# Optimization experiments

Measured on AMD Instinct MI355X. Metric: run time of the kernel, lower is better.

The kernel has to match this reference:

```python
import jax, jax.numpy as jnp
import numpy as np

EPS = 1e-7
K_IN, K_HID, K_OUT = 1.0, 1.1, 1.2
N_NODES, N_EDGES, IN_DIM, HID = 50000, 400000, 1024, 1024


def _expmap0(u, k):
    # u: tangent at origin with time component 0; u[:, 1:] are spatial coords
    sqrtK = jnp.sqrt(k)
    us = u[:, 1:]
    un = jnp.maximum(jnp.linalg.norm(us, axis=1, keepdims=True), EPS)
    t = un / sqrtK
    return jnp.concatenate([sqrtK * jnp.cosh(t), sqrtK * jnp.sinh(t) * us / un], axis=1)


def _logmap0(x, k):
    sqrtK = jnp.sqrt(k)
    x0, xs = x[:, 0:1], x[:, 1:]
    xn = jnp.maximum(jnp.linalg.norm(xs, axis=1, keepdims=True), EPS)
    theta = jnp.maximum(x0 / sqrtK, 1.0 + EPS)
    d = sqrtK * jnp.arccosh(theta)
    return jnp.concatenate([jnp.zeros_like(x0), d * xs / xn], axis=1)


def _proj(x, k):
    # re-fix the time component so <x,x>_L = -k
    xs = x[:, 1:]
    x0 = jnp.sqrt(k + jnp.sum(xs * xs, axis=1, keepdims=True))
    return jnp.concatenate([x0, xs], axis=1)


def _centroid(m, k):
    # Lorentzian centroid normalization: sqrt(k) * m / sqrt(|<m,m>_L|)
    l_inner = jnp.sum(m[:, 1:] ** 2, axis=1, keepdims=True) - m[:, 0:1] ** 2
    denom = jnp.sqrt(jnp.maximum(jnp.abs(l_inner), EPS))
    return jnp.sqrt(k) * m / denom


def _lgcn_conv(x, W, b, edge_src, edge_dst, edge_w, k_in, k_out):
    n = x.shape[0]
    # Lorentzian linear: logmap0 -> spatial matmul + bias -> expmap0
    u = _logmap0(x, k_in)[:, 1:]                      # [N, in_f]
    mx = u @ W.T + b                                  # [N, out_f-1]
    h = _expmap0(jnp.concatenate([jnp.zeros_like(mx[:, :1]), mx], axis=1), k_in)
    # sparse neighborhood aggregation + Lorentzian centroid
    msgs = edge_w[:, None] * h[edge_src]              # [E, out_f]
    m = jax.ops.segment_sum(msgs, edge_dst, num_segments=n)
    h = _centroid(m, k_in)
    # Lorentzian activation: relu in tangent space, re-exp on output manifold
    t = jax.nn.relu(_logmap0(h, k_in))                # time comp stays 0
    return _proj(_expmap0(t, k_out), k_out)


def setup_inputs() -> dict:
    key = jax.random.key(0)
    ks = jax.random.split(key, 8)
    x = jax.random.normal(ks[0], (N_NODES, IN_DIM), jnp.float32) * 0.01
    edge_src = jax.random.randint(ks[1], (N_EDGES,), 0, N_NODES, jnp.int32)
    edge_dst = jax.random.randint(ks[2], (N_EDGES,), 0, N_NODES, jnp.int32)
    edge_w = jax.random.uniform(ks[3], (N_EDGES,), jnp.float32)
    W1 = jax.random.normal(ks[4], (HID - 1, IN_DIM), jnp.float32) * 0.02
    b1 = jax.random.normal(ks[5], (HID - 1,), jnp.float32) * 0.01
    W2 = jax.random.normal(ks[6], (HID - 1, HID - 1), jnp.float32) * 0.02
    b2 = jax.random.normal(ks[7], (HID - 1,), jnp.float32) * 0.01
    return {"x": x, "edge_src": edge_src, "edge_dst": edge_dst, "edge_w": edge_w,
            "W1": W1, "b1": b1, "W2": W2, "b2": b2}


def reference(x, edge_src, edge_dst, edge_w, W1, b1, W2, b2):
    # encode(): prepend zero time coord, proj_tan0 (already 0), expmap0, proj
    x = jnp.concatenate([jnp.zeros_like(x[:, :1]), x], axis=1)  # [N, IN_DIM+1]
    xh = _proj(_expmap0(x, K_IN), K_IN)
    x1 = _lgcn_conv(xh, W1, b1, edge_src, edge_dst, edge_w, K_IN, K_HID)
    y = _lgcn_conv(x1, W2, b2, edge_src, edge_dst, edge_w, K_HID, K_OUT)
    return y
```

## Files before the change

### kernel.cpp

```cpp
#include <hip/hip_runtime.h>
#include <math.h>

#define EPSF 1e-7f
#define KPAD 1024
#define M_PAD 50176
#define NWG2 784

typedef __attribute__((ext_vector_type(8))) short bf16x8;
typedef __attribute__((ext_vector_type(4))) float f32x4;
typedef __attribute__((ext_vector_type(4))) unsigned short us4;
typedef __attribute__((ext_vector_type(8))) unsigned short us8;

__device__ inline unsigned short f2bf(float f) {
  unsigned u = __float_as_uint(f);
  return (unsigned short)((u + 0x7FFFu + ((u >> 16) & 1u)) >> 16);
}
__device__ inline float bf2f(unsigned short s) {
  return __uint_as_float(((unsigned)s) << 16);
}

__device__ inline float block_sum256(float v, float* s4) {
#pragma unroll
  for (int o = 32; o > 0; o >>= 1) v += __shfl_down(v, o);
  int lane = threadIdx.x & 63, w = threadIdx.x >> 6;
  __syncthreads();
  if (lane == 0) s4[w] = v;
  __syncthreads();
  return s4[0] + s4[1] + s4[2] + s4[3];
}

__device__ inline void gload_lds16(const void* g, void* l) {
  __builtin_amdgcn_global_load_lds((const __attribute__((address_space(1))) void*)g,
                                   (__attribute__((address_space(3))) void*)l, 16, 0, 0);
}

__global__ __launch_bounds__(256) void cvt_rows_bf16(const float* __restrict__ x,
                                                     unsigned short* __restrict__ o) {
  int i = blockIdx.x, t = threadIdx.x;
  float4 v = *(const float4*)(x + (size_t)i * 1024 + 4 * t);
  us4 u = {f2bf(v.x), f2bf(v.y), f2bf(v.z), f2bf(v.w)};
  *(us4*)(o + (size_t)i * 1024 + 4 * t) = u;
}

__global__ __launch_bounds__(256) void cvt_w_bf16(const float* __restrict__ W,
                                                  unsigned short* __restrict__ o,
                                                  int rows, int cols) {
  int r = blockIdx.x, t = threadIdx.x;
  int c0 = 4 * t;
  us4 u;
#pragma unroll
  for (int j = 0; j < 4; ++j) {
    int c = c0 + j;
    float v = (r < rows && c < cols) ? W[(size_t)r * cols + c] : 0.0f;
    u[j] = f2bf(v);
  }
  *(us4*)(o + (size_t)r * 1024 + c0) = u;
}

__global__ __launch_bounds__(512, 2) void gemm_bt256(const unsigned short* __restrict__ A,
                                                     const unsigned short* __restrict__ B,
                                                     const float* __restrict__ bias,
                                                     unsigned short* __restrict__ C) {
  __shared__ unsigned short lA[2 * 2 * 8192];
  __shared__ unsigned short lB[2 * 2 * 8192];
  const int wg = blockIdx.x;
  const int swz = (wg & 7) * 98 + (wg >> 3);
  const int bm = swz >> 2, bn = swz & 3;
  const int tid = threadIdx.x;
  const int wave = tid >> 6, lane = tid & 63;
  const int wr = wave >> 2, wc = wave & 3;
  const int fr = lane & 15, fg = lane >> 4;

  const unsigned short* Abase = A + (size_t)bm * 256 * KPAD;
  const unsigned short* Bbase = B + (size_t)bn * 256 * KPAD;

  const int aHalf = wr * 8192;
  const int bHalf = (wc >> 1) * 8192;
  const int lrB0 = (wc & 1) * 64;
  int ps[2];
#pragma unroll
  for (int s = 0; s < 2; ++s) ps[s] = (((s << 2) + fg) ^ (fr & 7)) << 3;

  const int sRow8 = lane >> 3;
  const int sDst = wave * 512 + lane * 8;
  const int sGran = ((lane & 7) ^ sRow8) << 3;

  f32x4 acc[8][4];
#pragma unroll
  for (int m = 0; m < 8; ++m)
#pragma unroll
    for (int n2 = 0; n2 < 4; ++n2) acc[m][n2] = (f32x4)0.0f;

  bf16x8 af[4][2], bf[4][2];

  auto STAGE_A = [&](int t, int h) {
    const int p = t & 1;
#pragma unroll
    for (int q = 0; q < 2; ++q) {
      int row = h * 128 + q * 64 + wave * 8 + sRow8;
      gload_lds16(Abase + (size_t)row * KPAD + t * 64 + sGran,
                  &lA[p * 16384 + h * 8192 + q * 4096 + sDst]);
    }
  };
  auto STAGE_B = [&](int t, int h) {
    const int p = t & 1;
#pragma unroll
    for (int q = 0; q < 2; ++q) {
      int row = h * 128 + q * 64 + wave * 8 + sRow8;
      gload_lds16(Bbase + (size_t)row * KPAD + t * 64 + sGran,
                  &lB[p * 16384 + h * 8192 + q * 4096 + sDst]);
    }
  };
  auto LDA4 = [&](int p, int mg) {
#pragma unroll
    for (int mi = 0; mi < 4; ++mi) {
      int ro = p * 16384 + aHalf + ((mg * 4 + mi) * 16 + fr) * 64;
#pragma unroll
      for (int s = 0; s < 2; ++s) af[mi][s] = *(const bf16x8*)&lA[ro + ps[s]];
    }
  };
  auto LDB2 = [&](int p, int ng) {
#pragma unroll
    for (int ni = 0; ni < 2; ++ni) {
      int ro = p * 16384 + bHalf + (lrB0 + (ng * 2 + ni) * 16 + fr) * 64;
#pragma unroll
      for (int s = 0; s < 2; ++s) bf[ng * 2 + ni][s] = *(const bf16x8*)&lB[ro + ps[s]];
    }
  };
  auto MM = [&](int mq, int nq) {
    __builtin_amdgcn_s_setprio(1);
#pragma unroll
    for (int mi = 0; mi < 4; ++mi)
#pragma unroll
      for (int ni = 0; ni < 2; ++ni)
#pragma unroll
        for (int s = 0; s < 2; ++s)
          acc[mq * 4 + mi][nq * 2 + ni] = __builtin_amdgcn_mfma_f32_16x16x32_bf16(
              af[mi][s], bf[nq * 2 + ni][s], acc[mq * 4 + mi][nq * 2 + ni], 0, 0, 0);
    __builtin_amdgcn_s_setprio(0);
  };
#define BAR() __builtin_amdgcn_s_barrier()

  STAGE_B(0, 0); STAGE_B(0, 1); STAGE_A(0, 0); STAGE_A(0, 1);
  STAGE_B(1, 0); STAGE_B(1, 1); STAGE_A(1, 0);
  asm volatile("s_waitcnt vmcnt(6)" ::: "memory");
  BAR();

#pragma unroll 1
  for (int it = 0; it < 7; ++it) {
    const int t0 = 2 * it, t1 = t0 + 1;
    LDA4(0, 0); LDB2(0, 0);
    STAGE_A(t1, 1);
    BAR(); MM(0, 0); BAR();
    LDB2(0, 1);
    BAR(); MM(0, 1); BAR();
    LDA4(0, 1);
    STAGE_B(t0 + 2, 0);
    BAR(); MM(1, 0); BAR();
    STAGE_B(t0 + 2, 1); STAGE_A(t0 + 2, 0);
    asm volatile("s_waitcnt vmcnt(6)" ::: "memory");
    BAR(); MM(1, 1); BAR();
    LDA4(1, 0); LDB2(1, 0);
    STAGE_A(t0 + 2, 1);
    BAR(); MM(0, 0); BAR();
    LDB2(1, 1);
    BAR(); MM(0, 1); BAR();
    LDA4(1, 1);
    STAGE_B(t1 + 2, 0);
    BAR(); MM(1, 0); BAR();
    STAGE_B(t1 + 2, 1); STAGE_A(t1 + 2, 0);
    asm volatile("s_waitcnt vmcnt(6)" ::: "memory");
    BAR(); MM(1, 1); BAR();
  }

  asm volatile("s_waitcnt vmcnt(0)" ::: "memory");
  BAR();
#pragma unroll
  for (int p = 0; p < 2; ++p) {
    LDA4(p, 0); LDB2(p, 0); MM(0, 0);
    LDB2(p, 1); MM(0, 1);
    LDA4(p, 1); MM(1, 0); MM(1, 1);
  }
#undef BAR

  const int crow0 = bm * 256 + wr * 128;
  const int ccol0 = bn * 256 + wc * 64;
#pragma unroll
  for (int m = 0; m < 8; ++m) {
#pragma unroll
    for (int n2 = 0; n2 < 4; ++n2) {
      int col = ccol0 + n2 * 16 + fr;
      float bv = (col < 1023) ? bias[col] : 0.0f;
      int row0 = crow0 + m * 16 + fg * 4;
      unsigned short* cp = C + (size_t)row0 * 1024 + col;
#pragma unroll
      for (int j = 0; j < 4; ++j) cp[(size_t)j * 1024] = f2bf(acc[m][n2][j] + bv);
    }
  }
}

__global__ __launch_bounds__(256) void row_scale(unsigned short* __restrict__ raw,
                                                 float* __restrict__ sc_tab, float sqrtK) {
  __shared__ float s4[4];
  int i = blockIdx.x, t = threadIdx.x;
  const us4 v = *(const us4*)(raw + (size_t)i * 1024 + 4 * t);
  float f0 = bf2f(v[0]), f1 = bf2f(v[1]), f2 = bf2f(v[2]), f3 = bf2f(v[3]);
  if (t == 255) f3 = 0.0f;
  float ss = block_sum256(f0 * f0 + f1 * f1 + f2 * f2 + f3 * f3, s4);
  float un = fmaxf(sqrtf(ss), EPSF);
  float tt = un / sqrtK;
  float e = expf(tt);
  float ch = 0.5f * (e + 1.0f / e), sh = 0.5f * (e - 1.0f / e);
  float h0 = sqrtK * ch, sc = sqrtK * sh / un;
  if (t == 0) sc_tab[i] = sc;
  if (t == 255) raw[(size_t)i * 1024 + 1023] = f2bf(h0 / sc);
}

__global__ __launch_bounds__(256) void deg_count(const int* __restrict__ ed, int* __restrict__ cnt,
                                                 int nE) {
  int i = blockIdx.x * 256 + threadIdx.x;
  if (i < nE) atomicAdd(&cnt[ed[i]], 1);
}

__global__ __launch_bounds__(256) void scan1(const int* __restrict__ cnt, int* __restrict__ excl,
                                             int* __restrict__ bsum, int n) {
  __shared__ int s[256];
  int t = threadIdx.x;
  int i = blockIdx.x * 256 + t;
  int v = (i < n) ? cnt[i] : 0;
  s[t] = v;
  __syncthreads();
#pragma unroll
  for (int o = 1; o < 256; o <<= 1) {
    int add = (t >= o) ? s[t - o] : 0;
    __syncthreads();
    s[t] += add;
    __syncthreads();
  }
  if (i < n) excl[i] = s[t] - v;
  if (t == 255) bsum[blockIdx.x] = s[t];
}

__global__ __launch_bounds__(256) void scan2(int* __restrict__ bsum, int* __restrict__ boff,
                                             int nb) {
  __shared__ int s[256];
  int t = threadIdx.x;
  int v = (t < nb) ? bsum[t] : 0;
  s[t] = v;
  __syncthreads();
#pragma unroll
  for (int o = 1; o < 256; o <<= 1) {
    int add = (t >= o) ? s[t - o] : 0;
    __syncthreads();
    s[t] += add;
    __syncthreads();
  }
  if (t < nb) boff[t] = s[t] - v;
}

__global__ __launch_bounds__(256) void scan3(int* __restrict__ excl, const int* __restrict__ boff,
                                             int* __restrict__ rowstart, int* __restrict__ fill,
                                             int n, int nE) {
  int i = blockIdx.x * 256 + threadIdx.x;
  if (i < n) {
    int v = excl[i] + boff[blockIdx.x];
    rowstart[i] = v;
    fill[i] = v;
  }
  if (i == 0) rowstart[n] = nE;
}

__global__ __launch_bounds__(256) void bucket_fill(const int* __restrict__ es,
                                                   const int* __restrict__ ed,
                                                   const float* __restrict__ ew,
                                                   int* __restrict__ fill,
                                                   int2* __restrict__ sedge, int nE) {
  int i = blockIdx.x * 256 + threadIdx.x;
  if (i < nE) {
    int d = ed[i];
    int pos = atomicAdd(&fill[d], 1);
    sedge[pos] = make_int2(es[i], __float_as_int(ew[i]));
  }
}

__device__ inline void gather_row(const unsigned short* __restrict__ h,
                                  const float* __restrict__ sc,
                                  const int2* __restrict__ sedge, int j0, int j1, int t,
                                  float* acc) {
  int j = j0;
  for (; j + 4 <= j1; j += 4) {
    int2 e0 = sedge[j], e1 = sedge[j + 1], e2 = sedge[j + 2], e3 = sedge[j + 3];
    float w0 = __int_as_float(e0.y) * sc[e0.x];
    float w1 = __int_as_float(e1.y) * sc[e1.x];
    float w2 = __int_as_float(e2.y) * sc[e2.x];
    float w3 = __int_as_float(e3.y) * sc[e3.x];
    us8 v0 = *(const us8*)(h + (size_t)e0.x * 1024 + 8 * t);
    us8 v1 = *(const us8*)(h + (size_t)e1.x * 1024 + 8 * t);
    us8 v2 = *(const us8*)(h + (size_t)e2.x * 1024 + 8 * t);
    us8 v3 = *(const us8*)(h + (size_t)e3.x * 1024 + 8 * t);
#pragma unroll
    for (int q = 0; q < 8; ++q) {
      acc[q] += w0 * bf2f(v0[q]);
      acc[q] += w1 * bf2f(v1[q]);
      acc[q] += w2 * bf2f(v2[q]);
      acc[q] += w3 * bf2f(v3[q]);
    }
  }
  for (; j < j1; ++j) {
    int2 e = sedge[j];
    float w = __int_as_float(e.y) * sc[e.x];
    us8 v = *(const us8*)(h + (size_t)e.x * 1024 + 8 * t);
#pragma unroll
    for (int q = 0; q < 8; ++q) acc[q] += w * bf2f(v[q]);
  }
}

__global__ __launch_bounds__(256) void gather_centroid_tangent(
    const unsigned short* __restrict__ h, const float* __restrict__ sc,
    const int* __restrict__ rs, const int2* __restrict__ sedge,
    unsigned short* __restrict__ u16, float sqrtK, int n) {
  __shared__ float s4[4];
  __shared__ float sm0[2];
  int g = threadIdx.x >> 7;
  int t = threadIdx.x & 127;
  int i = blockIdx.x * 2 + g;
  bool alive = (i < n);
  int j0 = alive ? rs[i] : 0, j1 = alive ? rs[i + 1] : 0;
  float acc[8] = {0.f, 0.f, 0.f, 0.f, 0.f, 0.f, 0.f, 0.f};
  gather_row(h, sc, sedge, j0, j1, t, acc);
  if (t == 127) sm0[g] = acc[7];
  __syncthreads();
  float m0 = sm0[g];
  if (t == 127) acc[7] = 0.0f;
  float ssl = 0.f;
#pragma unroll
  for (int q = 0; q < 8; ++q) ssl += acc[q] * acc[q];
#pragma unroll
  for (int o = 32; o > 0; o >>= 1) ssl += __shfl_down(ssl, o);
  int lane = threadIdx.x & 63, wv = threadIdx.x >> 6;
  if (lane == 0) s4[wv] = ssl;
  __syncthreads();
  float ss = s4[2 * g] + s4[2 * g + 1];

  float l = ss - m0 * m0;
  float denom = sqrtf(fmaxf(fabsf(l), EPSF));
  float c = sqrtK / denom;
  float xn = fmaxf(c * sqrtf(ss), EPSF);
  float theta = fmaxf(m0 / denom, 1.0f + EPSF);
  float d = sqrtK * acoshf(theta);
  float f = c * (d / xn);
  us8 u;
#pragma unroll
  for (int q = 0; q < 8; ++q) u[q] = f2bf(fmaxf(acc[q], 0.0f) * f);
  if (t == 127) u[7] = 0;
  if (alive) *(us8*)(u16 + (size_t)i * 1024 + 8 * t) = u;
}

__global__ __launch_bounds__(256) void gather_centroid_final(
    const unsigned short* __restrict__ h, const float* __restrict__ sc,
    const int* __restrict__ rs, const int2* __restrict__ sedge, float* __restrict__ y,
    float sqrtKin, float sqrtKout, int n) {
  __shared__ float s4[4];
  __shared__ float s4b[4];
  __shared__ float sm0[2];
  int g = threadIdx.x >> 7;
  int t = threadIdx.x & 127;
  int i = blockIdx.x * 2 + g;
  bool alive = (i < n);
  int j0 = alive ? rs[i] : 0, j1 = alive ? rs[i + 1] : 0;
  float acc[8] = {0.f, 0.f, 0.f, 0.f, 0.f, 0.f, 0.f, 0.f};
  gather_row(h, sc, sedge, j0, j1, t, acc);
  if (t == 127) sm0[g] = acc[7];
  __syncthreads();
  float m0 = sm0[g];
  if (t == 127) acc[7] = 0.0f;
  float ssl = 0.f;
#pragma unroll
  for (int q = 0; q < 8; ++q) ssl += acc[q] * acc[q];
#pragma unroll
  for (int o = 32; o > 0; o >>= 1) ssl += __shfl_down(ssl, o);
  int lane = threadIdx.x & 63, wv = threadIdx.x >> 6;
  if (lane == 0) s4[wv] = ssl;
  __syncthreads();
  float ss = s4[2 * g] + s4[2 * g + 1];

  float l = ss - m0 * m0;
  float denom = sqrtf(fmaxf(fabsf(l), EPSF));
  float c = sqrtKin / denom;
  float xn = fmaxf(c * sqrtf(ss), EPSF);
  float theta = fmaxf(m0 / denom, 1.0f + EPSF);
  float d = sqrtKin * acoshf(theta);
  float f = c * (d / xn);
  float o_[8];
#pragma unroll
  for (int q = 0; q < 8; ++q) o_[q] = fmaxf(acc[q], 0.0f) * f;
  if (t == 127) o_[7] = 0.0f;
  float ss2l = 0.f;
#pragma unroll
  for (int q = 0; q < 8; ++q) ss2l += o_[q] * o_[q];
#pragma unroll
  for (int o = 32; o > 0; o >>= 1) ss2l += __shfl_down(ss2l, o);
  if (lane == 0) s4b[wv] = ss2l;
  __syncthreads();
  float ss2 = s4b[2 * g] + s4b[2 * g + 1];

  float un = fmaxf(sqrtf(ss2), EPSF);
  float tt = un / sqrtKout;
  float e = expf(tt);
  float ch = 0.5f * (e + 1.0f / e), sh = 0.5f * (e - 1.0f / e);
  float y0 = sqrtKout * ch, scale = sqrtKout * sh / un;
  if (alive) {
    float* yr = y + (size_t)i * 1024;
    int c0 = 8 * t;
#pragma unroll
    for (int q = 0; q < 8; ++q) {
      int col = c0 + q;
      if (col < 1023) yr[1 + col] = scale * o_[q];
    }
    if (t == 0) yr[0] = y0;
  }
}

extern "C" void kernel_launch(void* const* d_in, const int* in_sizes, int n_in,
                              void* d_out, int out_size, void* d_ws, size_t ws_size,
                              hipStream_t stream) {
  const float* x = (const float*)d_in[0];
  const int* es = (const int*)d_in[1];
  const int* ed = (const int*)d_in[2];
  const float* ew = (const float*)d_in[3];
  const float* W1 = (const float*)d_in[4];
  const float* b1 = (const float*)d_in[5];
  const float* W2 = (const float*)d_in[6];
  const float* b2 = (const float*)d_in[7];
  float* y = (float*)d_out;

  const int n = in_sizes[0] / 1024;
  const int nE = in_sizes[1];
  const int NB = (n + 255) / 256;
  const int EB = (nE + 255) / 256;

  char* ws = (char*)d_ws;
  size_t off = 0;
  auto alloc = [&](size_t bytes) {
    void* p = ws + off;
    off += (bytes + 255) & ~(size_t)255;
    return p;
  };
  unsigned short* u16 = (unsigned short*)alloc((size_t)M_PAD * 1024 * 2);
  unsigned short* w16 = (unsigned short*)alloc((size_t)1024 * 1024 * 2);
  unsigned short* raw16 = (unsigned short*)alloc((size_t)M_PAD * 1024 * 2);
  float* sc_tab = (float*)alloc((size_t)M_PAD * 4);
  int* cnt = (int*)alloc((size_t)(n + 1) * 4);
  int* excl = (int*)alloc((size_t)n * 4);
  int* rowstart = (int*)alloc((size_t)(n + 1) * 4);
  int* fill = (int*)alloc((size_t)n * 4);
  int* bsum = (int*)alloc(256 * 4);
  int* boff = (int*)alloc(256 * 4);
  int2* sedge = (int2*)alloc((size_t)nE * 8);

  const float sK1 = 1.0f;
  const float sK2 = 1.0488088481701516f;
  const float sK3 = 1.0954451150103321f;

  const int GB = (n + 1) / 2;

  hipMemsetAsync(cnt, 0, (size_t)(n + 1) * 4, stream);
  deg_count<<<EB, 256, 0, stream>>>(ed, cnt, nE);
  scan1<<<NB, 256, 0, stream>>>(cnt, excl, bsum, n);
  scan2<<<1, 256, 0, stream>>>(bsum, boff, NB);
  scan3<<<NB, 256, 0, stream>>>(excl, boff, rowstart, fill, n, nE);
  bucket_fill<<<EB, 256, 0, stream>>>(es, ed, ew, fill, sedge, nE);

  cvt_rows_bf16<<<n, 256, 0, stream>>>(x, u16);
  cvt_w_bf16<<<1024, 256, 0, stream>>>(W1, w16, 1023, 1024);
  gemm_bt256<<<NWG2, 512, 0, stream>>>(u16, w16, b1, raw16);
  row_scale<<<n, 256, 0, stream>>>(raw16, sc_tab, sK1);
  gather_centroid_tangent<<<GB, 256, 0, stream>>>(raw16, sc_tab, rowstart, sedge, u16, sK1, n);

  cvt_w_bf16<<<1024, 256, 0, stream>>>(W2, w16, 1023, 1023);
  gemm_bt256<<<NWG2, 512, 0, stream>>>(u16, w16, b2, raw16);
  row_scale<<<n, 256, 0, stream>>>(raw16, sc_tab, sK2);
  gather_centroid_final<<<GB, 256, 0, stream>>>(raw16, sc_tab, rowstart, sedge, y, sK2, sK3, n);
}
```

Before: 715.6 us.

## Fuse row norm into GEMM epilogue and gather one row per wave

The GEMM epilogue now accumulates each output row's sum of squares in fp32. It reduces these across lanes and waves through LDS and writes per-column-block partials. A tiny per-row finalize kernel then replaces the full-row `row_scale` pass, removing a re-read of the whole bf16 intermediate after each GEMM. The gather kernels are also restructured so each wave handles one destination row with 16 columns per lane, using only wave shuffles and no `__syncthreads`. The trade-offs are extra registers and LDS traffic in the GEMM epilogue and a norm computed from unrounded values, which differs slightly from the old bf16-based one.

After: 686.2 us. -4.1%, faster.

```diff
diff --git a/kernel.cpp b/kernel.cpp
--- a/kernel.cpp
+++ b/kernel.cpp
@@ -17,16 +17,6 @@
 }
 __device__ inline float bf2f(unsigned short s) {
   return __uint_as_float(((unsigned)s) << 16);
-}
-
-__device__ inline float block_sum256(float v, float* s4) {
-#pragma unroll
-  for (int o = 32; o > 0; o >>= 1) v += __shfl_down(v, o);
-  int lane = threadIdx.x & 63, w = threadIdx.x >> 6;
-  __syncthreads();
-  if (lane == 0) s4[w] = v;
-  __syncthreads();
-  return s4[0] + s4[1] + s4[2] + s4[3];
 }
 
 __device__ inline void gload_lds16(const void* g, void* l) {
@@ -60,7 +50,8 @@
 __global__ __launch_bounds__(512, 2) void gemm_bt256(const unsigned short* __restrict__ A,
                                                      const unsigned short* __restrict__ B,
                                                      const float* __restrict__ bias,
-                                                     unsigned short* __restrict__ C) {
+                                                     unsigned short* __restrict__ C,
+                                                     float* __restrict__ rowss) {
   __shared__ unsigned short lA[2 * 2 * 8192];
   __shared__ unsigned short lB[2 * 2 * 8192];
   const int wg = blockIdx.x;
@@ -185,6 +176,11 @@
 
   const int crow0 = bm * 256 + wr * 128;
   const int ccol0 = bn * 256 + wc * 64;
+  float rs[8][4];
+#pragma unroll
+  for (int m = 0; m < 8; ++m)
+#pragma unroll
+    for (int j = 0; j < 4; ++j) rs[m][j] = 0.0f;
 #pragma unroll
   for (int m = 0; m < 8; ++m) {
 #pragma unroll
@@ -194,26 +190,54 @@
       int row0 = crow0 + m * 16 + fg * 4;
       unsigned short* cp = C + (size_t)row0 * 1024 + col;
 #pragma unroll
-      for (int j = 0; j < 4; ++j) cp[(size_t)j * 1024] = f2bf(acc[m][n2][j] + bv);
-    }
-  }
-}
-
-__global__ __launch_bounds__(256) void row_scale(unsigned short* __restrict__ raw,
-                                                 float* __restrict__ sc_tab, float sqrtK) {
-  __shared__ float s4[4];
-  int i = blockIdx.x, t = threadIdx.x;
-  const us4 v = *(const us4*)(raw + (size_t)i * 1024 + 4 * t);
-  float f0 = bf2f(v[0]), f1 = bf2f(v[1]), f2 = bf2f(v[2]), f3 = bf2f(v[3]);
-  if (t == 255) f3 = 0.0f;
-  float ss = block_sum256(f0 * f0 + f1 * f1 + f2 * f2 + f3 * f3, s4);
+      for (int j = 0; j < 4; ++j) {
+        float v = acc[m][n2][j] + bv;
+        cp[(size_t)j * 1024] = f2bf(v);
+        rs[m][j] += v * v;
+      }
+    }
+  }
+#pragma unroll
+  for (int m = 0; m < 8; ++m)
+#pragma unroll
+    for (int j = 0; j < 4; ++j) {
+      float v = rs[m][j];
+      v += __shfl_xor(v, 1);
+      v += __shfl_xor(v, 2);
+      v += __shfl_xor(v, 4);
+      v += __shfl_xor(v, 8);
+      rs[m][j] = v;
+    }
+  __syncthreads();
+  float* red = (float*)lA;
+  if (fr == 0) {
+#pragma unroll
+    for (int m = 0; m < 8; ++m)
+#pragma unroll
+      for (int j = 0; j < 4; ++j)
+        red[(wr * 128 + m * 16 + fg * 4 + j) * 4 + wc] = rs[m][j];
+  }
+  __syncthreads();
+  if (tid < 256) {
+    float s = red[tid * 4] + red[tid * 4 + 1] + red[tid * 4 + 2] + red[tid * 4 + 3];
+    rowss[(size_t)(bm * 256 + tid) * 4 + bn] = s;
+  }
+}
+
+__global__ __launch_bounds__(256) void row_finalize(const float* __restrict__ rowss,
+                                                    unsigned short* __restrict__ raw,
+                                                    float* __restrict__ sc_tab, float sqrtK,
+                                                    int n) {
+  int i = blockIdx.x * 256 + threadIdx.x;
+  if (i >= n) return;
+  float ss = rowss[4 * i] + rowss[4 * i + 1] + rowss[4 * i + 2] + rowss[4 * i + 3];
   float un = fmaxf(sqrtf(ss), EPSF);
   float tt = un / sqrtK;
   float e = expf(tt);
   float ch = 0.5f * (e + 1.0f / e), sh = 0.5f * (e - 1.0f / e);
   float h0 = sqrtK * ch, sc = sqrtK * sh / un;
-  if (t == 0) sc_tab[i] = sc;
-  if (t == 255) raw[(size_t)i * 1024 + 1023] = f2bf(h0 / sc);
+  sc_tab[i] = sc;
+  raw[(size_t)i * 1024 + 1023] = f2bf(h0 / sc);
 }
 
 __global__ __launch_bounds__(256) void deg_count(const int* __restrict__ ed, int* __restrict__ cnt,
@@ -283,64 +307,62 @@
   }
 }
 
-__device__ inline void gather_row(const unsigned short* __restrict__ h,
-                                  const float* __restrict__ sc,
-                                  const int2* __restrict__ sedge, int j0, int j1, int t,
-                                  float* acc) {
+__device__ inline void gather_row_wave(const unsigned short* __restrict__ h,
+                                       const float* __restrict__ sc,
+                                       const int2* __restrict__ sedge, int j0, int j1,
+                                       int lane, float* fa, float* fb) {
+  const char* hb = (const char*)h;
   int j = j0;
-  for (; j + 4 <= j1; j += 4) {
-    int2 e0 = sedge[j], e1 = sedge[j + 1], e2 = sedge[j + 2], e3 = sedge[j + 3];
+  for (; j + 2 <= j1; j += 2) {
+    int2 e0 = sedge[j], e1 = sedge[j + 1];
     float w0 = __int_as_float(e0.y) * sc[e0.x];
     float w1 = __int_as_float(e1.y) * sc[e1.x];
-    float w2 = __int_as_float(e2.y) * sc[e2.x];
-    float w3 = __int_as_float(e3.y) * sc[e3.x];
-    us8 v0 = *(const us8*)(h + (size_t)e0.x * 1024 + 8 * t);
-    us8 v1 = *(const us8*)(h + (size_t)e1.x * 1024 + 8 * t);
-    us8 v2 = *(const us8*)(h + (size_t)e2.x * 1024 + 8 * t);
-    us8 v3 = *(const us8*)(h + (size_t)e3.x * 1024 + 8 * t);
+    const us8* p0 = (const us8*)(hb + (((unsigned)e0.x) << 11)) + lane;
+    const us8* p1 = (const us8*)(hb + (((unsigned)e1.x) << 11)) + lane;
+    us8 a0 = p0[0], b0 = p0[64];
+    us8 a1 = p1[0], b1 = p1[64];
 #pragma unroll
     for (int q = 0; q < 8; ++q) {
-      acc[q] += w0 * bf2f(v0[q]);
-      acc[q] += w1 * bf2f(v1[q]);
-      acc[q] += w2 * bf2f(v2[q]);
-      acc[q] += w3 * bf2f(v3[q]);
-    }
-  }
-  for (; j < j1; ++j) {
+      fa[q] += w0 * bf2f(a0[q]) + w1 * bf2f(a1[q]);
+      fb[q] += w0 * bf2f(b0[q]) + w1 * bf2f(b1[q]);
+    }
+  }
+  if (j < j1) {
     int2 e = sedge[j];
     float w = __int_as_float(e.y) * sc[e.x];
-    us8 v = *(const us8*)(h + (size_t)e.x * 1024 + 8 * t);
-#pragma unroll
-    for (int q = 0; q < 8; ++q) acc[q] += w * bf2f(v[q]);
-  }
+    const us8* p = (const us8*)(hb + (((unsigned)e.x) << 11)) + lane;
+    us8 a = p[0], b = p[64];
+#pragma unroll
+    for (int q = 0; q < 8; ++q) {
+      fa[q] += w * bf2f(a[q]);
+      fb[q] += w * bf2f(b[q]);
+    }
+  }
+}
+
+__device__ inline float wave_sum(float v) {
+#pragma unroll
+  for (int m = 1; m <= 32; m <<= 1) v += __shfl_xor(v, m);
+  return v;
 }
 
 __global__ __launch_bounds__(256) void gather_centroid_tangent(
     const unsigned short* __restrict__ h, const float* __restrict__ sc,
     const int* __restrict__ rs, const int2* __restrict__ sedge,
     unsigned short* __restrict__ u16, float sqrtK, int n) {
-  __shared__ float s4[4];
-  __shared__ float sm0[2];
-  int g = threadIdx.x >> 7;
-  int t = threadIdx.x & 127;
-  int i = blockIdx.x * 2 + g;
-  bool alive = (i < n);
-  int j0 = alive ? rs[i] : 0, j1 = alive ? rs[i + 1] : 0;
-  float acc[8] = {0.f, 0.f, 0.f, 0.f, 0.f, 0.f, 0.f, 0.f};
-  gather_row(h, sc, sedge, j0, j1, t, acc);
-  if (t == 127) sm0[g] = acc[7];
-  __syncthreads();
-  float m0 = sm0[g];
-  if (t == 127) acc[7] = 0.0f;
+  int wv = threadIdx.x >> 6, lane = threadIdx.x & 63;
+  int i = blockIdx.x * 4 + wv;
+  if (i >= n) return;
+  int j0 = rs[i], j1 = rs[i + 1];
+  float fa[8] = {0.f, 0.f, 0.f, 0.f, 0.f, 0.f, 0.f, 0.f};
+  float fb[8] = {0.f, 0.f, 0.f, 0.f, 0.f, 0.f, 0.f, 0.f};
+  gather_row_wave(h, sc, sedge, j0, j1, lane, fa, fb);
+  float m0 = __shfl(fb[7], 63);
+  if (lane == 63) fb[7] = 0.0f;
   float ssl = 0.f;
 #pragma unroll
-  for (int q = 0; q < 8; ++q) ssl += acc[q] * acc[q];
-#pragma unroll
-  for (int o = 32; o > 0; o >>= 1) ssl += __shfl_down(ssl, o);
-  int lane = threadIdx.x & 63, wv = threadIdx.x >> 6;
-  if (lane == 0) s4[wv] = ssl;
-  __syncthreads();
-  float ss = s4[2 * g] + s4[2 * g + 1];
+  for (int q = 0; q < 8; ++q) ssl += fa[q] * fa[q] + fb[q] * fb[q];
+  float ss = wave_sum(ssl);
 
   float l = ss - m0 * m0;
   float denom = sqrtf(fmaxf(fabsf(l), EPSF));
@@ -349,40 +371,35 @@
   float theta = fmaxf(m0 / denom, 1.0f + EPSF);
   float d = sqrtK * acoshf(theta);
   float f = c * (d / xn);
-  us8 u;
-#pragma unroll
-  for (int q = 0; q < 8; ++q) u[q] = f2bf(fmaxf(acc[q], 0.0f) * f);
-  if (t == 127) u[7] = 0;
-  if (alive) *(us8*)(u16 + (size_t)i * 1024 + 8 * t) = u;
+  us8 ua, ub;
+#pragma unroll
+  for (int q = 0; q < 8; ++q) {
+    ua[q] = f2bf(fmaxf(fa[q], 0.0f) * f);
+    ub[q] = f2bf(fmaxf(fb[q], 0.0f) * f);
+  }
+  if (lane == 63) ub[7] = 0;
+  unsigned short* o = u16 + (size_t)i * 1024 + lane * 8;
+  *(us8*)o = ua;
+  *(us8*)(o + 512) = ub;
 }
 
 __global__ __launch_bounds__(256) void gather_centroid_final(
     const unsigned short* __restrict__ h, const float* __restrict__ sc,
     const int* __restrict__ rs, const int2* __restrict__ sedge, float* __restrict__ y,
     float sqrtKin, float sqrtKout, int n) {
-  __shared__ float s4[4];
-  __shared__ float s4b[4];
-  __shared__ float sm0[2];
-  int g = threadIdx.x >> 7;
-  int t = threadIdx.x & 127;
-  int i = blockIdx.x * 2 + g;
-  bool alive = (i < n);
-  int j0 = alive ? rs[i] : 0, j1 = alive ? rs[i + 1] : 0;
-  float acc[8] = {0.f, 0.f, 0.f, 0.f, 0.f, 0.f, 0.f, 0.f};
-  gather_row(h, sc, sedge, j0, j1, t, acc);
-  if (t == 127) sm0[g] = acc[7];
-  __syncthreads();
-  float m0 = sm0[g];
-  if (t == 127) acc[7] = 0.0f;
+  int wv = threadIdx.x >> 6, lane = threadIdx.x & 63;
+  int i = blockIdx.x * 4 + wv;
+  if (i >= n) return;
+  int j0 = rs[i], j1 = rs[i + 1];
+  float fa[8] = {0.f, 0.f, 0.f, 0.f, 0.f, 0.f, 0.f, 0.f};
+  float fb[8] = {0.f, 0.f, 0.f, 0.f, 0.f, 0.f, 0.f, 0.f};
+  gather_row_wave(h, sc, sedge, j0, j1, lane, fa, fb);
+  float m0 = __shfl(fb[7], 63);
+  if (lane == 63) fb[7] = 0.0f;
   float ssl = 0.f;
 #pragma unroll
-  for (int q = 0; q < 8; ++q) ssl += acc[q] * acc[q];
-#pragma unroll
-  for (int o = 32; o > 0; o >>= 1) ssl += __shfl_down(ssl, o);
-  int lane = threadIdx.x & 63, wv = threadIdx.x >> 6;
-  if (lane == 0) s4[wv] = ssl;
-  __syncthreads();
-  float ss = s4[2 * g] + s4[2 * g + 1];
+  for (int q = 0; q < 8; ++q) ssl += fa[q] * fa[q] + fb[q] * fb[q];
+  float ss = wave_sum(ssl);
 
   float l = ss - m0 * m0;
   float denom = sqrtf(fmaxf(fabsf(l), EPSF));
@@ -391,34 +408,32 @@
   float theta = fmaxf(m0 / denom, 1.0f + EPSF);
   float d = sqrtKin * acoshf(theta);
   float f = c * (d / xn);
-  float o_[8];
-#pragma unroll
-  for (int q = 0; q < 8; ++q) o_[q] = fmaxf(acc[q], 0.0f) * f;
-  if (t == 127) o_[7] = 0.0f;
+  float oa[8], ob[8];
   float ss2l = 0.f;
 #pragma unroll
-  for (int q = 0; q < 8; ++q) ss2l += o_[q] * o_[q];
-#pragma unroll
-  for (int o = 32; o > 0; o >>= 1) ss2l += __shfl_down(ss2l, o);
-  if (lane == 0) s4b[wv] = ss2l;
-  __syncthreads();
-  float ss2 = s4b[2 * g] + s4b[2 * g + 1];
+  for (int q = 0; q < 8; ++q) {
+    oa[q] = fmaxf(fa[q], 0.0f) * f;
+    ob[q] = fmaxf(fb[q], 0.0f) * f;
+  }
+  if (lane == 63) ob[7] = 0.0f;
+#pragma unroll
+  for (int q = 0; q < 8; ++q) ss2l += oa[q] * oa[q] + ob[q] * ob[q];
+  float ss2 = wave_sum(ss2l);
 
   float un = fmaxf(sqrtf(ss2), EPSF);
   float tt = un / sqrtKout;
   float e = expf(tt);
   float ch = 0.5f * (e + 1.0f / e), sh = 0.5f * (e - 1.0f / e);
   float y0 = sqrtKout * ch, scale = sqrtKout * sh / un;
-  if (alive) {
-    float* yr = y + (size_t)i * 1024;
-    int c0 = 8 * t;
-#pragma unroll
-    for (int q = 0; q < 8; ++q) {
-      int col = c0 + q;
-      if (col < 1023) yr[1 + col] = scale * o_[q];
-    }
-    if (t == 0) yr[0] = y0;
-  }
+  float* yr = y + (size_t)i * 1024;
+  int c0 = lane * 8;
+#pragma unroll
+  for (int q = 0; q < 8; ++q) {
+    yr[1 + c0 + q] = scale * oa[q];
+    int colb = 512 + c0 + q;
+    if (colb < 1023) yr[1 + colb] = scale * ob[q];
+  }
+  if (lane == 0) yr[0] = y0;
 }
 
 extern "C" void kernel_launch(void* const* d_in, const int* in_sizes, int n_in,
@@ -450,6 +465,7 @@
   unsigned short* w16 = (unsigned short*)alloc((size_t)1024 * 1024 * 2);
   unsigned short* raw16 = (unsigned short*)alloc((size_t)M_PAD * 1024 * 2);
   float* sc_tab = (float*)alloc((size_t)M_PAD * 4);
+  float* rowss = (float*)alloc((size_t)M_PAD * 4 * 4);
   int* cnt = (int*)alloc((size_t)(n + 1) * 4);
   int* excl = (int*)alloc((size_t)n * 4);
   int* rowstart = (int*)alloc((size_t)(n + 1) * 4);
@@ -462,7 +478,7 @@
   const float sK2 = 1.0488088481701516f;
   const float sK3 = 1.0954451150103321f;
 
-  const int GB = (n + 1) / 2;
+  const int GB = (n + 3) / 4;
 
   hipMemsetAsync(cnt, 0, (size_t)(n + 1) * 4, stream);
   deg_count<<<EB, 256, 0, stream>>>(ed, cnt, nE);
@@ -473,12 +489,12 @@
 
   cvt_rows_bf16<<<n, 256, 0, stream>>>(x, u16);
   cvt_w_bf16<<<1024, 256, 0, stream>>>(W1, w16, 1023, 1024);
-  gemm_bt256<<<NWG2, 512, 0, stream>>>(u16, w16, b1, raw16);
-  row_scale<<<n, 256, 0, stream>>>(raw16, sc_tab, sK1);
+  gemm_bt256<<<NWG2, 512, 0, stream>>>(u16, w16, b1, raw16, rowss);
+  row_finalize<<<NB, 256, 0, stream>>>(rowss, raw16, sc_tab, sK1, n);
   gather_centroid_tangent<<<GB, 256, 0, stream>>>(raw16, sc_tab, rowstart, sedge, u16, sK1, n);
 
   cvt_w_bf16<<<1024, 256, 0, stream>>>(W2, w16, 1023, 1023);
-  gemm_bt256<<<NWG2, 512, 0, stream>>>(u16, w16, b2, raw16);
-  row_scale<<<n, 256, 0, stream>>>(raw16, sc_tab, sK2);
+  gemm_bt256<<<NWG2, 512, 0, stream>>>(u16, w16, b2, raw16, rowss);
+  row_finalize<<<NB, 256, 0, stream>>>(rowss, raw16, sc_tab, sK2, n);
   gather_centroid_final<<<GB, 256, 0, stream>>>(raw16, sc_tab, rowstart, sedge, y, sK2, sK3, n);
 }
```
